# Kernel tuning notes

Measured on AMD Instinct MI355X. Metric: run time of the kernel, lower is better.

Reference implementation:

```python
import jax, jax.numpy as jnp
import numpy as np

V = 25   # NTU joints
NE = 5   # number of hyper-edge types


def setup_inputs() -> dict:
    key = jax.random.key(0)
    ks = jax.random.split(key, 8)
    N, C, T = 64, 12, 300
    x = jax.random.normal(ks[0], (N, C, T, V), dtype=jnp.float32)
    # binary incidence matrices [V, E] with E == V, as in the NTU hyper-edge tables
    hs = [jax.random.bernoulli(ks[1 + i], 0.2, (V, V)).astype(jnp.float32) for i in range(NE)]
    in_ch, out_ch = 3, 64
    w_mlp = jax.random.normal(ks[6], (out_ch, in_ch * NE), dtype=jnp.float32) * (1.0 / np.sqrt(in_ch * NE))
    b_mlp = jnp.zeros((out_ch,), dtype=jnp.float32)
    return {"x": x, "h_local": hs[0], "h_center": hs[1], "h_figl": hs[2],
            "h_figr": hs[3], "h_hand": hs[4], "w_mlp": w_mlp, "b_mlp": b_mlp}


def _normalized_aggregate(w, h):
    # w: [N, T, E], h: [V, E] (E == V)
    degree_v = jnp.einsum('ve,bte->btv', h, w)
    # pow(d, -0.5): inf at d==0 and nan at d<0 are both zeroed in the original
    dv_pos = degree_v > 0
    degree_v = jnp.where(dv_pos, jax.lax.rsqrt(jnp.where(dv_pos, degree_v, 1.0)), 0.0)
    degree_e = jnp.sum(h, axis=0)                      # [E]
    de_nz = degree_e != 0
    degree_e = jnp.where(de_nz, 1.0 / jnp.where(de_nz, degree_e, 1.0), 0.0)
    # fused dh * w * degree_e chain: [N, T, V, E]
    dhwb = degree_v[..., None] * h[None, None] * w[:, :, None, :] * degree_e
    dhwbht = jnp.einsum('btve,ue->btvu', dhwb, h)      # [N, T, V, V]
    return dhwbht * degree_v[:, :, None, :]


def reference(x, h_local, h_center, h_figl, h_figr, h_hand, w_mlp, b_mlp):
    ws = (x[:, 6], x[:, 7], x[:, 9], x[:, 10], x[:, 11])
    hs = (h_local, h_center, h_figl, h_figr, h_hand)
    hwh_cat = jnp.concatenate([_normalized_aggregate(w, h) for w, h in zip(ws, hs)], axis=-2)  # [N,T,5V,V]
    feat = x[:, :3]                                    # [N, 3, T, V]
    N, C, T, Vv = feat.shape
    support = jnp.einsum('btvu,bctu->bctv', hwh_cat, feat)          # [N, C, T, 5V]
    support = support.reshape(N, C, T, NE, Vv).transpose(0, 3, 1, 2, 4).reshape(N, NE * C, T, Vv)
    out = jnp.einsum('oi,bitv->botv', w_mlp, support) + b_mlp[None, :, None, None]
    return jax.nn.relu(out)
```

## Files before the change

kernel.cpp:

```cpp
#include <hip/hip_runtime.h>

#define NE  5
#define V   25
#define NT  300
#define NC  12
#define CO  64
#define WPB 4
#define GX  38

typedef float f4 __attribute__((ext_vector_type(4)));

#define WSYNC() do { asm volatile("s_waitcnt lgkmcnt(0)" ::: "memory"); \
                     __builtin_amdgcn_sched_barrier(0); } while (0)

__device__ __forceinline__ float hsel(unsigned m, int e, float w) {
    int s = ((int)(m << (31 - e))) >> 31;
    return __int_as_float(__float_as_int(w) & s);
}

#define OW   0
#define ODV  224
#define OG   364
#define OB   504
#define OFP  924
#define OST  1344
#define SCRF 2364

#define STROW(r) (OST + (r)*20 + (((r) >> 3) & 7)*4)

__global__ __launch_bounds__(256, 4) void hyper_main(
    const float* __restrict__ x,
    const float* __restrict__ h0, const float* __restrict__ h1,
    const float* __restrict__ h2, const float* __restrict__ h3,
    const float* __restrict__ h4,
    const float* __restrict__ wmlp, const float* __restrict__ bmlp,
    float* __restrict__ out)
{
    __shared__ unsigned RM[125];
    __shared__ unsigned CM[125];
    __shared__ float    DE[125];
    __shared__ __align__(16) float SCR[WPB][SCRF];

    const int tid  = threadIdx.x;
    const int lane = tid & 63;
    const int wid  = tid >> 6;
    const int b    = blockIdx.y;

    if (tid < 125) {
        int i = tid / 25, v = tid % 25;
        const float* hp = (i==0)?h0:(i==1)?h1:(i==2)?h2:(i==3)?h3:h4;
        unsigned m = 0;
        for (int e = 0; e < V; ++e) if (hp[v*V + e] != 0.f) m |= (1u << e);
        RM[tid] = m;
    } else if (tid < 250) {
        int idx = tid - 125, i = idx / 25, e = idx % 25;
        const float* hp = (i==0)?h0:(i==1)?h1:(i==2)?h2:(i==3)?h3:h4;
        unsigned m = 0; float s = 0.f;
        for (int u = 0; u < V; ++u) {
            float hv = hp[u*V + e];
            s += hv;
            if (hv != 0.f) m |= (1u << u);
        }
        CM[idx] = m;
        DE[idx] = (s != 0.f) ? __fdiv_rn(1.f, s) : 0.f;
    }
    __syncthreads();

    const int pp = blockIdx.x * WPB + wid;
    if (pp >= NT/2) return;

    float* S = SCR[wid];

    const float* xb[4]; int lo[4];
    {
        #pragma unroll
        for (int r = 0; r < 4; ++r) {
            int q  = r*64 + lane;
            int qq = (q < 200) ? q : 0;
            int ch = qq / 25, e = qq % 25;
            int xc = (ch < 5) ? (ch + 6 + (ch >= 2 ? 1 : 0)) : (ch - 5);
            lo[r] = OW + ch*28 + e;
            xb[r] = x + (size_t)(b*NC + xc)*NT*V + e;
        }
    }
    const bool act3 = (lane < 8);

    float pf0, pf1, pf2, pf3;
    {
        int t0 = 2 * pp;
        pf0 = xb[0][t0*V]; pf1 = xb[1][t0*V];
        pf2 = xb[2][t0*V]; pf3 = xb[3][t0*V];
    }

    for (int tp = 0; tp < 2; ++tp) {

        S[lo[0]] = pf0; S[lo[1]] = pf1; S[lo[2]] = pf2;
        if (act3) S[lo[3]] = pf3;
        WSYNC();

        if (tp == 0) {
            int tn = 2*pp + 1;
            pf0 = xb[0][tn*V]; pf1 = xb[1][tn*V];
            pf2 = xb[2][tn*V]; pf3 = xb[3][tn*V];
        }

        for (int r = 0; r < 2; ++r) {
            int idx = r*64 + lane;
            if (idx < 125) {
                int i = idx / 25, v = idx % 25;
                unsigned m = RM[idx];
                const float* wi = S + OW + i*28;
                f4 w0 = *(const f4*)(wi+0),  w1 = *(const f4*)(wi+4),
                   w2 = *(const f4*)(wi+8),  w3 = *(const f4*)(wi+12),
                   w4 = *(const f4*)(wi+16), w5 = *(const f4*)(wi+20),
                   w6 = *(const f4*)(wi+24);
                float L0 = 0.f, L1 = 0.f, L2 = 0.f, L3 = 0.f;
                L0=__fadd_rn(L0,hsel(m, 0,w0.x)); L1=__fadd_rn(L1,hsel(m, 1,w0.y));
                L2=__fadd_rn(L2,hsel(m, 2,w0.z)); L3=__fadd_rn(L3,hsel(m, 3,w0.w));
                L0=__fadd_rn(L0,hsel(m, 4,w1.x)); L1=__fadd_rn(L1,hsel(m, 5,w1.y));
                L2=__fadd_rn(L2,hsel(m, 6,w1.z)); L3=__fadd_rn(L3,hsel(m, 7,w1.w));
                L0=__fadd_rn(L0,hsel(m, 8,w2.x)); L1=__fadd_rn(L1,hsel(m, 9,w2.y));
                L2=__fadd_rn(L2,hsel(m,10,w2.z)); L3=__fadd_rn(L3,hsel(m,11,w2.w));
                L0=__fadd_rn(L0,hsel(m,12,w3.x)); L1=__fadd_rn(L1,hsel(m,13,w3.y));
                L2=__fadd_rn(L2,hsel(m,14,w3.z)); L3=__fadd_rn(L3,hsel(m,15,w3.w));
                L0=__fadd_rn(L0,hsel(m,16,w4.x)); L1=__fadd_rn(L1,hsel(m,17,w4.y));
                L2=__fadd_rn(L2,hsel(m,18,w4.z)); L3=__fadd_rn(L3,hsel(m,19,w4.w));
                L0=__fadd_rn(L0,hsel(m,20,w5.x)); L1=__fadd_rn(L1,hsel(m,21,w5.y));
                L2=__fadd_rn(L2,hsel(m,22,w5.z)); L3=__fadd_rn(L3,hsel(m,23,w5.w));
                float s = __fadd_rn(__fadd_rn(L0,L1), __fadd_rn(L2,L3));
                s = __fadd_rn(s, hsel(m, 24, w6.x));
                float dvv = (s > 0.f) ? (float)(1.0 / sqrt((double)s)) : 0.f;
                S[ODV + i*28 + v] = dvv;
                S[OG  + i*28 + v] = S[OW + i*28 + v] * DE[idx];
                float f0 = S[OW + 5*28 + v];
                float f1 = S[OW + 6*28 + v];
                float f2v = S[OW + 7*28 + v];
                S[OB + (0*5+i)*28 + v] = dvv * f0;
                S[OB + (1*5+i)*28 + v] = dvv * f1;
                S[OB + (2*5+i)*28 + v] = dvv * f2v;
            }
        }
        WSYNC();

        for (int r = 0; r < 2; ++r) {
            int idx = r*64 + lane;
            if (idx < 125) {
                int i = idx / 25, e = idx % 25;
                unsigned m = CM[idx];
                const float* bp = S + OB + i*28;
                float a0 = 0.f, a1 = 0.f, a2 = 0.f;
                while (m) {
                    int u[5]; bool vl[5];
                    #pragma unroll
                    for (int j = 0; j < 5; ++j) {
                        vl[j] = (m != 0u);
                        u[j]  = __builtin_ctz(m | 0x02000000u);
                        m &= m - 1;
                    }
                    float b0[5], b1[5], b2[5];
                    #pragma unroll
                    for (int j = 0; j < 5; ++j) {
                        b0[j] = bp[u[j]];
                        b1[j] = bp[140 + u[j]];
                        b2[j] = bp[280 + u[j]];
                    }
                    #pragma unroll
                    for (int j = 0; j < 5; ++j) {
                        a0 += vl[j] ? b0[j] : 0.f;
                        a1 += vl[j] ? b1[j] : 0.f;
                        a2 += vl[j] ? b2[j] : 0.f;
                    }
                }
                float gg = S[OG + i*28 + e];
                S[OFP + (i*3+0)*28 + e] = a0 * gg;
                S[OFP + (i*3+1)*28 + e] = a1 * gg;
                S[OFP + (i*3+2)*28 + e] = a2 * gg;
            }
        }
        WSYNC();

        for (int r = 0; r < 2; ++r) {
            int idx = r*64 + lane;
            if (idx < 125) {
                int i = idx / 25, v = idx % 25;
                unsigned m = RM[idx];
                const float* fp = S + OFP + i*3*28;
                float a0 = 0.f, a1 = 0.f, a2 = 0.f;
                while (m) {
                    int u[5]; bool vl[5];
                    #pragma unroll
                    for (int j = 0; j < 5; ++j) {
                        vl[j] = (m != 0u);
                        u[j]  = __builtin_ctz(m | 0x02000000u);
                        m &= m - 1;
                    }
                    float b0[5], b1[5], b2[5];
                    #pragma unroll
                    for (int j = 0; j < 5; ++j) {
                        b0[j] = fp[u[j]];
                        b1[j] = fp[28 + u[j]];
                        b2[j] = fp[56 + u[j]];
                    }
                    #pragma unroll
                    for (int j = 0; j < 5; ++j) {
                        a0 += vl[j] ? b0[j] : 0.f;
                        a1 += vl[j] ? b1[j] : 0.f;
                        a2 += vl[j] ? b2[j] : 0.f;
                    }
                }
                float dd = S[ODV + i*28 + v];
                float* st = S + STROW(tp*25 + v) + i*3;
                st[0] = a0 * dd; st[1] = a1 * dd; st[2] = a2 * dd;
            }
        }
        WSYNC();
    }

    if (lane < 50) {
        const float* st = S + STROW(lane);
        f4 s0 = *(const f4*)(st+0), s1 = *(const f4*)(st+4),
           s2 = *(const f4*)(st+8), s3 = *(const f4*)(st+12);
        s3.w = 0.f;
        float* ob = out + (size_t)b*CO*7500 + (size_t)pp*50 + lane;
        #pragma unroll 8
        for (int o = 0; o < CO; ++o) {
            const float* wm = wmlp + o*15;
            float a = bmlp[o];
            a = fmaf(wm[ 0], s0.x, a); a = fmaf(wm[ 1], s0.y, a);
            a = fmaf(wm[ 2], s0.z, a); a = fmaf(wm[ 3], s0.w, a);
            a = fmaf(wm[ 4], s1.x, a); a = fmaf(wm[ 5], s1.y, a);
            a = fmaf(wm[ 6], s1.z, a); a = fmaf(wm[ 7], s1.w, a);
            a = fmaf(wm[ 8], s2.x, a); a = fmaf(wm[ 9], s2.y, a);
            a = fmaf(wm[10], s2.z, a); a = fmaf(wm[11], s2.w, a);
            a = fmaf(wm[12], s3.x, a); a = fmaf(wm[13], s3.y, a);
            a = fmaf(wm[14], s3.z, a);
            __builtin_nontemporal_store(fmaxf(a, 0.f), ob + (size_t)o*7500);
        }
    }
}

extern "C" void kernel_launch(void* const* d_in, const int* in_sizes, int n_in,
                              void* d_out, int out_size, void* d_ws, size_t ws_size,
                              hipStream_t stream) {
    const float* x    = (const float*)d_in[0];
    const float* h0   = (const float*)d_in[1];
    const float* h1   = (const float*)d_in[2];
    const float* h2   = (const float*)d_in[3];
    const float* h3   = (const float*)d_in[4];
    const float* h4   = (const float*)d_in[5];
    const float* wmlp = (const float*)d_in[6];
    const float* bmlp = (const float*)d_in[7];
    float* out = (float*)d_out;

    hyper_main<<<dim3(GX, 64, 1), dim3(256,1,1), 0, stream>>>(
        x, h0, h1, h2, h3, h4, wmlp, bmlp, out);
}
```

Measured before the change: 67.08 us.

## Redistribute MLP epilogue across block waves with paired-column vectorized stores

The output MLP stage used to run per wave, each wave producing all 64 output channels for its own 50 time-vertex columns. It now waits on a block-wide barrier and splits the channels across the 4 waves (16 each). Each lane handles two adjacent columns taken from any wave's scratch, computing with packed float2 arithmetic and writing 8-byte stores. Out-of-range waves stay alive with clamped loads so the barrier is legal, at the cost of an extra __syncthreads and dropping the nontemporal store hint.

```diff
diff --git a/kernel.cpp b/kernel.cpp
--- a/kernel.cpp
+++ b/kernel.cpp
@@ -9,6 +9,7 @@
 #define GX  38
 
 typedef float f4 __attribute__((ext_vector_type(4)));
+typedef float f2 __attribute__((ext_vector_type(2)));
 
 #define WSYNC() do { asm volatile("s_waitcnt lgkmcnt(0)" ::: "memory"); \
                      __builtin_amdgcn_sched_barrier(0); } while (0)
@@ -67,7 +68,7 @@
     __syncthreads();
 
     const int pp = blockIdx.x * WPB + wid;
-    if (pp >= NT/2) return;
+    const bool wvalid = (pp < NT/2);
 
     float* S = SCR[wid];
 
@@ -87,7 +88,7 @@
 
     float pf0, pf1, pf2, pf3;
     {
-        int t0 = 2 * pp;
+        int t0 = wvalid ? 2 * pp : 0;
         pf0 = xb[0][t0*V]; pf1 = xb[1][t0*V];
         pf2 = xb[2][t0*V]; pf3 = xb[3][t0*V];
     }
@@ -99,7 +100,7 @@
         WSYNC();
 
         if (tp == 0) {
-            int tn = 2*pp + 1;
+            int tn = wvalid ? (2*pp + 1) : 0;
             pf0 = xb[0][tn*V]; pf1 = xb[1][tn*V];
             pf2 = xb[2][tn*V]; pf3 = xb[3][tn*V];
         }
@@ -216,25 +217,46 @@
         WSYNC();
     }
 
+    __syncthreads();
+
     if (lane < 50) {
-        const float* st = S + STROW(lane);
-        f4 s0 = *(const f4*)(st+0), s1 = *(const f4*)(st+4),
-           s2 = *(const f4*)(st+8), s3 = *(const f4*)(st+12);
-        s3.w = 0.f;
-        float* ob = out + (size_t)b*CO*7500 + (size_t)pp*50 + lane;
-        #pragma unroll 8
-        for (int o = 0; o < CO; ++o) {
-            const float* wm = wmlp + o*15;
-            float a = bmlp[o];
-            a = fmaf(wm[ 0], s0.x, a); a = fmaf(wm[ 1], s0.y, a);
-            a = fmaf(wm[ 2], s0.z, a); a = fmaf(wm[ 3], s0.w, a);
-            a = fmaf(wm[ 4], s1.x, a); a = fmaf(wm[ 5], s1.y, a);
-            a = fmaf(wm[ 6], s1.z, a); a = fmaf(wm[ 7], s1.w, a);
-            a = fmaf(wm[ 8], s2.x, a); a = fmaf(wm[ 9], s2.y, a);
-            a = fmaf(wm[10], s2.z, a); a = fmaf(wm[11], s2.w, a);
-            a = fmaf(wm[12], s3.x, a); a = fmaf(wm[13], s3.y, a);
-            a = fmaf(wm[14], s3.z, a);
-            __builtin_nontemporal_store(fmaxf(a, 0.f), ob + (size_t)o*7500);
+        const int o0 = wid * 16;
+        #pragma unroll
+        for (int g = 0; g < 2; ++g) {
+            int q  = 2*g + (lane >= 25 ? 1 : 0);
+            int rr = (lane >= 25) ? 2*(lane - 25) : 2*lane;
+            const float* SQ = SCR[q];
+            const float* ra = SQ + STROW(rr);
+            const float* rb = SQ + STROW(rr + 1);
+            f4 a0 = *(const f4*)(ra+0), a1 = *(const f4*)(ra+4),
+               a2 = *(const f4*)(ra+8), a3 = *(const f4*)(ra+12);
+            f4 b0 = *(const f4*)(rb+0), b1 = *(const f4*)(rb+4),
+               b2 = *(const f4*)(rb+8), b3 = *(const f4*)(rb+12);
+            f2 k0 = {a0.x, b0.x}, k1 = {a0.y, b0.y}, k2 = {a0.z, b0.z},
+               k3 = {a0.w, b0.w}, k4 = {a1.x, b1.x}, k5 = {a1.y, b1.y},
+               k6 = {a1.z, b1.z}, k7 = {a1.w, b1.w}, k8 = {a2.x, b2.x},
+               k9 = {a2.y, b2.y}, k10 = {a2.z, b2.z}, k11 = {a2.w, b2.w},
+               k12 = {a3.x, b3.x}, k13 = {a3.y, b3.y}, k14 = {a3.z, b3.z};
+            int pg = blockIdx.x*200 + q*50 + rr;
+            bool ok = (pg < 7500);
+            float* ob = out + (size_t)b*CO*7500 + pg;
+            #pragma unroll 4
+            for (int oi = 0; oi < 16; ++oi) {
+                int o = o0 + oi;
+                const float* wm = wmlp + o*15;
+                float bb = bmlp[o];
+                f2 acc = {bb, bb};
+                acc += k0  * wm[ 0]; acc += k1  * wm[ 1];
+                acc += k2  * wm[ 2]; acc += k3  * wm[ 3];
+                acc += k4  * wm[ 4]; acc += k5  * wm[ 5];
+                acc += k6  * wm[ 6]; acc += k7  * wm[ 7];
+                acc += k8  * wm[ 8]; acc += k9  * wm[ 9];
+                acc += k10 * wm[10]; acc += k11 * wm[11];
+                acc += k12 * wm[12]; acc += k13 * wm[13];
+                acc += k14 * wm[14];
+                f2 res = {fmaxf(acc.x, 0.f), fmaxf(acc.y, 0.f)};
+                if (ok) *(f2*)(ob + (size_t)o*7500) = res;
+            }
         }
     }
 }
```

New measurement: 78.57 us. +17.1%, slower.
